# Kernel optimization log

Hardware: AMD Instinct MI355X
Metric: run time of the kernel (lower is better)

The kernel has to match this reference:

```python
import jax, jax.numpy as jnp
import numpy as np

NUM_CLASSES = 22
SKIP = 20            # skip_pixels: stride over flattened pixel index
N_STEPS = 200        # discretized steps along each voting ray
STEP = 4.0           # pixels per ray step
INLIER_T = 0.9       # inlier_threshold on direction dot-product
LABEL_T = 500.0      # label_threshold: min #pixels of a class to be valid


def _hough_forward(label_2d, vertex_pred, extents, poses, meta_data):
    B, H, W = label_2d.shape
    C = NUM_CLASSES
    HW = H * W

    # ---- strided pixel sampling (skip_pixels) ----
    idx = jnp.arange(0, HW, SKIP)                      # [P]
    P = idx.shape[0]
    ys = (idx // W).astype(jnp.float32)                # [P]
    xs = (idx % W).astype(jnp.float32)
    labels = label_2d.reshape(B, HW)[:, idx].astype(jnp.int32)   # [B,P]
    vp = vertex_pred.reshape(B, HW, C, 3)[:, idx]                # [B,P,C,3]
    # pick each pixel's predicted (dx,dy,z) for its own class label
    sel = jnp.take_along_axis(
        vp, jnp.broadcast_to(labels[:, :, None, None], (B, P, 1, 3)), axis=2
    )[:, :, 0]                                                   # [B,P,3]
    d = sel[..., :2]
    dn = d / (jnp.linalg.norm(d, axis=-1, keepdims=True) + 1e-9)  # unit dir [B,P,2]
    z = sel[..., 2]                                               # [B,P]
    fg = labels > 0                                               # foreground mask

    # ---- ray voting into per-class Hough accumulator ----
    t = (jnp.arange(N_STEPS, dtype=jnp.float32) + 1.0) * STEP     # [T]
    cx = xs[None, :, None] + dn[..., 0:1] * t[None, None, :]      # [B,P,T]
    cy = ys[None, :, None] + dn[..., 1:2] * t[None, None, :]
    cxi = jnp.round(cx).astype(jnp.int32)
    cyi = jnp.round(cy).astype(jnp.int32)
    inb = (cxi >= 0) & (cxi < W) & (cyi >= 0) & (cyi < H) & fg[..., None]
    cxi = jnp.clip(cxi, 0, W - 1)
    cyi = jnp.clip(cyi, 0, H - 1)
    bidx = jnp.arange(B, dtype=jnp.int32)[:, None, None]
    flat = ((bidx * C + labels[:, :, None]) * H + cyi) * W + cxi  # [B,P,T]
    hough = jnp.zeros((B * C * HW,), jnp.float32)
    hough = hough.at[flat.reshape(-1)].add(inb.reshape(-1).astype(jnp.float32))
    hough = hough.reshape(B, C, H, W)

    # ---- per-class peak ----
    hflat = hough.reshape(B, C, HW)
    vmax = hflat.max(-1)                               # [B,C]
    pk = jnp.argmax(hflat, axis=-1).astype(jnp.int32)  # [B,C]
    pky = (pk // W).astype(jnp.float32)
    pkx = (pk % W).astype(jnp.float32)

    # ---- validity: enough labeled pixels for the class ----
    b2 = jnp.arange(B, dtype=jnp.int32)[:, None]
    counts = jnp.zeros((B, C), jnp.float32).at[
        jnp.broadcast_to(b2, (B, HW)).reshape(-1),
        label_2d.reshape(-1).astype(jnp.int32),
    ].add(1.0)                                          # [B,C] full-res pixel counts
    cls_ids = jnp.arange(C, dtype=jnp.float32)
    valid = (counts >= LABEL_T) & (cls_ids[None, :] > 0)  # [B,C]

    # ---- inlier selection + inlier-averaged depth ----
    cx_c = jnp.take_along_axis(pkx, labels, axis=1)    # [B,P] peak of pixel's class
    cy_c = jnp.take_along_axis(pky, labels, axis=1)
    dvec = jnp.stack([cx_c - xs[None, :], cy_c - ys[None, :]], axis=-1)
    dvec = dvec / (jnp.linalg.norm(dvec, axis=-1, keepdims=True) + 1e-9)
    dot = jnp.sum(dn * dvec, axis=-1)                  # [B,P]
    inl = (fg & (dot > INLIER_T)).astype(jnp.float32)  # [B,P]
    bP = jnp.broadcast_to(b2, (B, P)).reshape(-1)
    z_sum = jnp.zeros((B, C), jnp.float32).at[bP, labels.reshape(-1)].add((z * inl).reshape(-1))
    n_inl = jnp.zeros((B, C), jnp.float32).at[bP, labels.reshape(-1)].add(inl.reshape(-1))
    depth = z_sum / jnp.maximum(n_inl, 1.0)            # [B,C]
    z_safe = jnp.where(jnp.abs(depth) > 1e-3, depth, 1.0)

    # ---- bbox from extents + intrinsics ----
    fx = meta_data[:, 0:1]                             # [B,1]
    fy = meta_data[:, 4:5]
    diam = jnp.linalg.norm(extents, axis=-1)[None, :]  # [1,C]
    half_w = 0.5 * diam * fx / z_safe
    half_h = 0.5 * diam * fy / z_safe
    vmask = valid.astype(jnp.float32)
    rois = jnp.stack([
        jnp.broadcast_to(b2.astype(jnp.float32), (B, C)),
        jnp.broadcast_to(cls_ids[None, :], (B, C)),
        pkx - half_w, pky - half_h, pkx + half_w, pky + half_h,
        vmax,
    ], axis=-1) * vmask[..., None]                     # [B,C,7]

    # ---- pose init: identity quaternion + backprojected translation ----
    Kinv = meta_data[:, 9:18].reshape(B, 3, 3)
    hom = jnp.stack([pkx, pky, jnp.ones_like(pkx)], axis=-1)      # [B,C,3]
    ray = jnp.einsum('bij,bcj->bci', Kinv, hom)
    T = depth[..., None] * ray                                    # [B,C,3]
    quat = jnp.broadcast_to(jnp.array([1.0, 0.0, 0.0, 0.0], jnp.float32), (B, C, 4))
    pose_out = jnp.concatenate([quat, T], axis=-1) * vmask[..., None]  # [B,C,7]

    return jnp.concatenate([rois, pose_out], axis=-1)  # [B,C,14]


def setup_inputs() -> dict:
    key = jax.random.key(0)
    k1, k2, k3 = jax.random.split(key, 3)
    B, H, W = 2, 480, 640
    label_2d = jax.random.randint(k1, (B, H, W), 0, NUM_CLASSES, dtype=jnp.int32)
    vertex_pred = jax.random.normal(k2, (B, H, W, 3 * NUM_CLASSES), dtype=jnp.float32)
    extents = jax.random.uniform(k3, (NUM_CLASSES, 3), minval=0.05, maxval=0.3, dtype=jnp.float32)
    poses = jnp.zeros((B, 13), jnp.float32)
    K = np.array([[1066.778, 0, 312.9869], [0, 1067.487, 241.3109], [0, 0, 1]], dtype=np.float32)
    Kinv = np.linalg.pinv(K).astype(np.float32)
    md = np.zeros((B, 48), np.float32)
    md[:, 0:9] = K.flatten()
    md[:, 9:18] = Kinv.flatten()
    meta_data = jnp.asarray(md)
    return {"label_2d": label_2d, "vertex_pred": vertex_pred, "extents": extents,
            "poses": poses, "meta_data": meta_data}


def reference(label_2d, vertex_pred, extents, poses, meta_data):
    return _hough_forward(label_2d, vertex_pred, extents, poses, meta_data)
```

## Files before the change

kernel.cpp:

```cpp
#include <hip/hip_runtime.h>
#include <math.h>

#define C_      22
#define SKIP_   20
#define NSTEP_  200
#define STEP_   4.0f
#define INL_T_  0.9f
#define LAB_T_  500
#define B_      2
#define H_      480
#define W_      640
#define HW_     (H_ * W_)
#define P_      (HW_ / SKIP_)

#define TS_       64
#define TILES_X_  (W_ / TS_)
#define TILES_Y_  (H_ / TS_)
#define NTILES_Y_ 8
#define NTILES_   (TILES_X_ * NTILES_Y_)
#define NPLANES_  (B_ * (C_ - 1))
#define NPT_      (NPLANES_ * NTILES_)
#define CAP_      1024

#define SUB_A_    4
#define SEG_LEN_  (NSTEP_ / SUB_A_)
#define PA_BLOCKS_    ((B_ * P_ * SUB_A_) / 256)
#define COUNT_BLOCKS_ ((B_ * HW_) / 256)

__device__ __forceinline__ void emit_run(unsigned int* cnt, uint4* lists, int pt,
                                         int xi, int yi, int i0, int i1,
                                         float dnx, float dny) {
    unsigned slot = atomicAdd(&cnt[pt], 1u);
    if (slot < CAP_) {
        uint4 r;
        r.x = (unsigned)xi | ((unsigned)yi << 16);
        r.y = (unsigned)i0 | ((unsigned)i1 << 8);
        r.z = __float_as_uint(dnx);
        r.w = __float_as_uint(dny);
        lists[(size_t)pt * CAP_ + slot] = r;
    }
}

__global__ __launch_bounds__(256) void binray_count_kernel(const int* __restrict__ label,
                                                           const float* __restrict__ vp,
                                                           unsigned int* __restrict__ cnt,
                                                           uint4* __restrict__ lists,
                                                           int* __restrict__ counts) {
    if (blockIdx.x < PA_BLOCKS_) {
        int tid = blockIdx.x * 256 + threadIdx.x;
        int pt  = tid >> 2;
        int sub = tid & 3;
        int b   = pt / P_;
        int pi  = pt - b * P_;
        int idx = pi * SKIP_;
        int lab = label[b * HW_ + idx];
        if (lab <= 0) return;
        int xi = idx % W_, yi = idx / W_;
        float xs = (float)xi, ys = (float)yi;
        const float* s = vp + ((size_t)(b * HW_ + idx) * (C_ * 3)) + lab * 3;
        float dx = s[0], dy = s[1];
        float nrm = sqrtf(__fadd_rn(__fmul_rn(dx, dx), __fmul_rn(dy, dy))) + 1e-9f;
        float dnx = dx / nrm, dny = dy / nrm;
        int base = (b * (C_ - 1) + (lab - 1)) * NTILES_;
        int curTile = -1, runStart = 0;
        int iBeg = sub * SEG_LEN_, iEnd = iBeg + SEG_LEN_;
        for (int i = iBeg; i < iEnd; ++i) {
            float t = (float)(i + 1) * STEP_;
            float cx = __fadd_rn(xs, __fmul_rn(dnx, t));
            float cy = __fadd_rn(ys, __fmul_rn(dny, t));
            float cxr = rintf(cx);
            float cyr = rintf(cy);
            int tile = -1;
            if (cxr >= 0.0f && cxr <= (float)(W_ - 1) && cyr >= 0.0f && cyr <= (float)(H_ - 1))
                tile = (((int)cyr) >> 6) * TILES_X_ + (((int)cxr) >> 6);
            if (tile != curTile) {
                if (curTile >= 0)
                    emit_run(cnt, lists, base + curTile, xi, yi, runStart, i - 1, dnx, dny);
                curTile = tile;
                runStart = i;
            }
        }
        if (curTile >= 0)
            emit_run(cnt, lists, base + curTile, xi, yi, runStart, iEnd - 1, dnx, dny);
    } else {
        __shared__ int h[C_];
        int cb  = blockIdx.x - PA_BLOCKS_;
        const int bpb = HW_ / 256;
        int b   = cb / bpb;
        int off = (cb % bpb) * 256 + threadIdx.x;
        if (threadIdx.x < C_) h[threadIdx.x] = 0;
        __syncthreads();
        int lab = label[b * HW_ + off];
        atomicAdd(&h[lab], 1);
        __syncthreads();
        if (threadIdx.x < C_) {
            int v = h[threadIdx.x];
            if (v) atomicAdd(&counts[b * C_ + threadIdx.x], v);
        }
    }
}

__global__ __launch_bounds__(256) void raster_argmax_kernel(const unsigned int* __restrict__ cnt,
                                                            const uint4* __restrict__ lists,
                                                            unsigned long long* __restrict__ key) {
    __shared__ unsigned int tile[TS_ * TS_];
    __shared__ unsigned int sv[256];
    __shared__ int          si[256];
    int ptile = blockIdx.x;
    int p  = ptile / NTILES_;
    int tl = ptile % NTILES_;
    int b = p / (C_ - 1);
    int c = p % (C_ - 1) + 1;
    int x0 = (tl % TILES_X_) * TS_;
    int y0 = (tl / TILES_X_) * TS_;
    for (int j = threadIdx.x; j < TS_ * TS_; j += 256) tile[j] = 0u;
    __syncthreads();
    int n = (int)cnt[ptile];
    if (n > CAP_) n = CAP_;
    const uint4* lst = lists + (size_t)ptile * CAP_;
    int wave = threadIdx.x >> 6, lane = threadIdx.x & 63;
    for (int r = wave; r < n; r += 4) {
        uint4 rec = lst[r];
        int i0 = (int)(rec.y & 0xFFu), i1 = (int)((rec.y >> 8) & 0xFFu);
        int i = i0 + lane;
        if (i <= i1) {
            float xs = (float)(rec.x & 0xFFFFu);
            float ys = (float)(rec.x >> 16);
            float dnx = __uint_as_float(rec.z);
            float dny = __uint_as_float(rec.w);
            float t = (float)(i + 1) * STEP_;
            float cx = __fadd_rn(xs, __fmul_rn(dnx, t));
            float cy = __fadd_rn(ys, __fmul_rn(dny, t));
            int lx = (int)rintf(cx) - x0;
            int ly = (int)rintf(cy) - y0;
            atomicAdd(&tile[ly * TS_ + lx], 1u);
        }
    }
    __syncthreads();
    int start = threadIdx.x * 16;
    unsigned bv = tile[start];
    int bloc = start;
    #pragma unroll
    for (int j = 1; j < 16; ++j) {
        unsigned v = tile[start + j];
        if (v > bv) { bv = v; bloc = start + j; }
    }
    sv[threadIdx.x] = bv; si[threadIdx.x] = bloc;
    __syncthreads();
    for (int s = 128; s > 0; s >>= 1) {
        if (threadIdx.x < s) {
            unsigned ov = sv[threadIdx.x + s]; int oi = si[threadIdx.x + s];
            if (ov > sv[threadIdx.x] || (ov == sv[threadIdx.x] && oi < si[threadIdx.x])) {
                sv[threadIdx.x] = ov; si[threadIdx.x] = oi;
            }
        }
        __syncthreads();
    }
    if (threadIdx.x == 0) {
        int ly = si[0] >> 6, lx = si[0] & 63;
        unsigned gidx = (unsigned)((y0 + ly) * W_ + (x0 + lx));
        unsigned long long k = ((unsigned long long)sv[0] << 32)
                             | (unsigned long long)(0xFFFFFFFFu - gidx);
        atomicMax(&key[b * C_ + c], k);
    }
}

__global__ __launch_bounds__(256) void inlier_kernel(const int* __restrict__ label,
                                                     const float* __restrict__ vp,
                                                     const unsigned long long* __restrict__ key,
                                                     float* __restrict__ z_sum,
                                                     float* __restrict__ n_inl) {
    __shared__ float zs[C_];
    __shared__ float ns[C_];
    const int bpb = P_ / 256;
    int b  = blockIdx.x / bpb;
    int pi = (blockIdx.x % bpb) * 256 + threadIdx.x;
    if (threadIdx.x < C_) { zs[threadIdx.x] = 0.0f; ns[threadIdx.x] = 0.0f; }
    __syncthreads();
    int idx = pi * SKIP_;
    int lab = label[b * HW_ + idx];
    if (lab > 0) {
        float ys = (float)(idx / W_);
        float xs = (float)(idx % W_);
        const float* s = vp + ((size_t)(b * HW_ + idx) * (C_ * 3)) + lab * 3;
        float dx = s[0], dy = s[1], z = s[2];
        float nrm = sqrtf(__fadd_rn(__fmul_rn(dx, dx), __fmul_rn(dy, dy))) + 1e-9f;
        float dnx = dx / nrm, dny = dy / nrm;
        unsigned long long k = key[b * C_ + lab];
        int pkv = (int)(0xFFFFFFFFu - (unsigned int)(k & 0xFFFFFFFFull));
        float pkx = (float)(pkv % W_), pky = (float)(pkv / W_);
        float dvx = __fsub_rn(pkx, xs), dvy = __fsub_rn(pky, ys);
        float nrm2 = sqrtf(__fadd_rn(__fmul_rn(dvx, dvx), __fmul_rn(dvy, dvy))) + 1e-9f;
        dvx /= nrm2; dvy /= nrm2;
        float dot = __fadd_rn(__fmul_rn(dnx, dvx), __fmul_rn(dny, dvy));
        if (dot > INL_T_) {
            atomicAdd(&zs[lab], z);
            atomicAdd(&ns[lab], 1.0f);
        }
    }
    __syncthreads();
    if (threadIdx.x < C_) {
        if (ns[threadIdx.x] != 0.0f) {
            atomicAdd(&z_sum[b * C_ + threadIdx.x], zs[threadIdx.x]);
            atomicAdd(&n_inl[b * C_ + threadIdx.x], ns[threadIdx.x]);
        }
    }
}

__global__ __launch_bounds__(64) void finalize_kernel(const int* __restrict__ counts,
                                                      const unsigned long long* __restrict__ key,
                                                      const float* __restrict__ z_sum,
                                                      const float* __restrict__ n_inl,
                                                      const float* __restrict__ extents,
                                                      const float* __restrict__ meta,
                                                      float* __restrict__ out) {
    int t = threadIdx.x;
    if (t >= B_ * C_) return;
    int b = t / C_, c = t % C_;
    float* o = out + t * 14;
    bool valid = (counts[t] >= LAB_T_) && (c > 0);
    if (!valid) {
        #pragma unroll
        for (int k = 0; k < 14; ++k) o[k] = 0.0f;
        return;
    }
    float depth = z_sum[t] / fmaxf(n_inl[t], 1.0f);
    float z_safe = (fabsf(depth) > 0.001f) ? depth : 1.0f;
    float fx = meta[b * 48 + 0];
    float fy = meta[b * 48 + 4];
    const float* e = extents + c * 3;
    float diam = sqrtf(e[0]*e[0] + e[1]*e[1] + e[2]*e[2]);
    unsigned long long k = key[t];
    float vmax = (float)(unsigned int)(k >> 32);
    int pkv = (int)(0xFFFFFFFFu - (unsigned int)(k & 0xFFFFFFFFull));
    float pkx = (float)(pkv % W_), pky = (float)(pkv / W_);
    float half_w = ((0.5f * diam) * fx) / z_safe;
    float half_h = ((0.5f * diam) * fy) / z_safe;
    o[0] = (float)b;
    o[1] = (float)c;
    o[2] = pkx - half_w;
    o[3] = pky - half_h;
    o[4] = pkx + half_w;
    o[5] = pky + half_h;
    o[6] = vmax;
    const float* Ki = meta + b * 48 + 9;
    float rx = Ki[0]*pkx + Ki[1]*pky + Ki[2];
    float ry = Ki[3]*pkx + Ki[4]*pky + Ki[5];
    float rz = Ki[6]*pkx + Ki[7]*pky + Ki[8];
    o[7]  = 1.0f;
    o[8]  = 0.0f;
    o[9]  = 0.0f;
    o[10] = 0.0f;
    o[11] = depth * rx;
    o[12] = depth * ry;
    o[13] = depth * rz;
}

extern "C" void kernel_launch(void* const* d_in, const int* in_sizes, int n_in,
                              void* d_out, int out_size, void* d_ws, size_t ws_size,
                              hipStream_t stream) {
    const int*   label   = (const int*)d_in[0];
    const float* vp      = (const float*)d_in[1];
    const float* extents = (const float*)d_in[2];
    const float* meta    = (const float*)d_in[4];
    float* out = (float*)d_out;

    char* ws = (char*)d_ws;
    size_t off = 0;
    unsigned int* cnt = (unsigned int*)(ws + off);          off += NPT_ * sizeof(unsigned int);
    unsigned long long* key = (unsigned long long*)(ws + off); off += B_ * C_ * sizeof(unsigned long long);
    int*   counts = (int*)(ws + off);   off += B_ * C_ * sizeof(int);
    float* z_sum  = (float*)(ws + off); off += B_ * C_ * sizeof(float);
    float* n_inl  = (float*)(ws + off); off += B_ * C_ * sizeof(float);
    size_t zero_bytes = off;
    uint4* lists = (uint4*)(ws + off);

    hipMemsetAsync(d_ws, 0, zero_bytes, stream);

    binray_count_kernel<<<PA_BLOCKS_ + COUNT_BLOCKS_, 256, 0, stream>>>(label, vp, cnt, lists, counts);
    raster_argmax_kernel<<<NPT_, 256, 0, stream>>>(cnt, lists, key);
    inlier_kernel<<<(B_ * P_) / 256, 256, 0, stream>>>(label, vp, key, z_sum, n_inl);
    finalize_kernel<<<1, 64, 0, stream>>>(counts, key, z_sum, n_inl, extents, meta, out);
}
```

Before: 288.1 us.

## Fuse memset and four kernels into one cooperative persistent kernel with grid syncs

Replaces the memset and the four separate launches (ray binning plus label counting, tile raster argmax, inlier accumulation, finalize) with one cooperative kernel of 512 persistent blocks. The blocks zero the workspace themselves and separate the phases with grid.sync. This removes launch and inter-kernel gaps, at the cost of grid barriers and a fixed block count that limits parallelism in the binning phase. The raster phase also changes from 64-lane waves per record to 32-lane groups with a strided loop, and the argmax scan changes from contiguous to strided shared-memory reads.

```diff
diff --git a/kernel.cpp b/kernel.cpp
--- a/kernel.cpp
+++ b/kernel.cpp
@@ -1,5 +1,8 @@
 #include <hip/hip_runtime.h>
+#include <hip/hip_cooperative_groups.h>
 #include <math.h>
+
+namespace cg = cooperative_groups;
 
 #define C_      22
 #define SKIP_   20
@@ -15,7 +18,6 @@
 
 #define TS_       64
 #define TILES_X_  (W_ / TS_)
-#define TILES_Y_  (H_ / TS_)
 #define NTILES_Y_ 8
 #define NTILES_   (TILES_X_ * NTILES_Y_)
 #define NPLANES_  (B_ * (C_ - 1))
@@ -26,6 +28,8 @@
 #define SEG_LEN_  (NSTEP_ / SUB_A_)
 #define PA_BLOCKS_    ((B_ * P_ * SUB_A_) / 256)
 #define COUNT_BLOCKS_ ((B_ * HW_) / 256)
+#define NB_       512
+#define ZERO_WORDS_ 13660
 
 __device__ __forceinline__ void emit_run(unsigned int* cnt, uint4* lists, int pt,
                                          int xi, int yi, int i0, int i1,
@@ -41,219 +45,226 @@
     }
 }
 
-__global__ __launch_bounds__(256) void binray_count_kernel(const int* __restrict__ label,
-                                                           const float* __restrict__ vp,
-                                                           unsigned int* __restrict__ cnt,
-                                                           uint4* __restrict__ lists,
-                                                           int* __restrict__ counts) {
-    if (blockIdx.x < PA_BLOCKS_) {
-        int tid = blockIdx.x * 256 + threadIdx.x;
-        int pt  = tid >> 2;
-        int sub = tid & 3;
-        int b   = pt / P_;
-        int pi  = pt - b * P_;
-        int idx = pi * SKIP_;
-        int lab = label[b * HW_ + idx];
-        if (lab <= 0) return;
-        int xi = idx % W_, yi = idx / W_;
-        float xs = (float)xi, ys = (float)yi;
-        const float* s = vp + ((size_t)(b * HW_ + idx) * (C_ * 3)) + lab * 3;
-        float dx = s[0], dy = s[1];
-        float nrm = sqrtf(__fadd_rn(__fmul_rn(dx, dx), __fmul_rn(dy, dy))) + 1e-9f;
-        float dnx = dx / nrm, dny = dy / nrm;
-        int base = (b * (C_ - 1) + (lab - 1)) * NTILES_;
-        int curTile = -1, runStart = 0;
-        int iBeg = sub * SEG_LEN_, iEnd = iBeg + SEG_LEN_;
-        for (int i = iBeg; i < iEnd; ++i) {
-            float t = (float)(i + 1) * STEP_;
-            float cx = __fadd_rn(xs, __fmul_rn(dnx, t));
-            float cy = __fadd_rn(ys, __fmul_rn(dny, t));
-            float cxr = rintf(cx);
-            float cyr = rintf(cy);
-            int tile = -1;
-            if (cxr >= 0.0f && cxr <= (float)(W_ - 1) && cyr >= 0.0f && cyr <= (float)(H_ - 1))
-                tile = (((int)cyr) >> 6) * TILES_X_ + (((int)cxr) >> 6);
-            if (tile != curTile) {
-                if (curTile >= 0)
-                    emit_run(cnt, lists, base + curTile, xi, yi, runStart, i - 1, dnx, dny);
-                curTile = tile;
-                runStart = i;
-            }
-        }
-        if (curTile >= 0)
-            emit_run(cnt, lists, base + curTile, xi, yi, runStart, iEnd - 1, dnx, dny);
-    } else {
-        __shared__ int h[C_];
-        int cb  = blockIdx.x - PA_BLOCKS_;
-        const int bpb = HW_ / 256;
-        int b   = cb / bpb;
-        int off = (cb % bpb) * 256 + threadIdx.x;
-        if (threadIdx.x < C_) h[threadIdx.x] = 0;
-        __syncthreads();
-        int lab = label[b * HW_ + off];
-        atomicAdd(&h[lab], 1);
-        __syncthreads();
-        if (threadIdx.x < C_) {
-            int v = h[threadIdx.x];
-            if (v) atomicAdd(&counts[b * C_ + threadIdx.x], v);
-        }
-    }
-}
-
-__global__ __launch_bounds__(256) void raster_argmax_kernel(const unsigned int* __restrict__ cnt,
-                                                            const uint4* __restrict__ lists,
-                                                            unsigned long long* __restrict__ key) {
+__global__ __launch_bounds__(256) void fused_kernel(
+        const int* __restrict__ label, const float* __restrict__ vp,
+        const float* __restrict__ extents, const float* __restrict__ meta,
+        float* __restrict__ out,
+        unsigned int* __restrict__ cnt, uint4* __restrict__ lists,
+        int* __restrict__ counts, unsigned long long* __restrict__ key,
+        float* __restrict__ z_sum, float* __restrict__ n_inl,
+        unsigned int* __restrict__ zero_base) {
+    cg::grid_group grid = cg::this_grid();
     __shared__ unsigned int tile[TS_ * TS_];
     __shared__ unsigned int sv[256];
     __shared__ int          si[256];
-    int ptile = blockIdx.x;
-    int p  = ptile / NTILES_;
-    int tl = ptile % NTILES_;
-    int b = p / (C_ - 1);
-    int c = p % (C_ - 1) + 1;
-    int x0 = (tl % TILES_X_) * TS_;
-    int y0 = (tl / TILES_X_) * TS_;
-    for (int j = threadIdx.x; j < TS_ * TS_; j += 256) tile[j] = 0u;
-    __syncthreads();
-    int n = (int)cnt[ptile];
-    if (n > CAP_) n = CAP_;
-    const uint4* lst = lists + (size_t)ptile * CAP_;
-    int wave = threadIdx.x >> 6, lane = threadIdx.x & 63;
-    for (int r = wave; r < n; r += 4) {
-        uint4 rec = lst[r];
-        int i0 = (int)(rec.y & 0xFFu), i1 = (int)((rec.y >> 8) & 0xFFu);
-        int i = i0 + lane;
-        if (i <= i1) {
+    __shared__ int   h[C_];
+    __shared__ float zs[C_], ns[C_];
+
+    int gtid = blockIdx.x * 256 + threadIdx.x;
+    if (gtid < ZERO_WORDS_) zero_base[gtid] = 0u;
+    grid.sync();
+
+    for (int vb = blockIdx.x; vb < PA_BLOCKS_ + COUNT_BLOCKS_; vb += NB_) {
+        if (vb < PA_BLOCKS_) {
+            int tid = vb * 256 + threadIdx.x;
+            int pt  = tid >> 2;
+            int sub = tid & 3;
+            int b   = pt / P_;
+            int pi  = pt - b * P_;
+            int idx = pi * SKIP_;
+            int lab = label[b * HW_ + idx];
+            if (lab > 0) {
+                int xi = idx % W_, yi = idx / W_;
+                float xs = (float)xi, ys = (float)yi;
+                const float* s = vp + ((size_t)(b * HW_ + idx) * (C_ * 3)) + lab * 3;
+                float dx = s[0], dy = s[1];
+                float nrm = sqrtf(__fadd_rn(__fmul_rn(dx, dx), __fmul_rn(dy, dy))) + 1e-9f;
+                float dnx = dx / nrm, dny = dy / nrm;
+                int base = (b * (C_ - 1) + (lab - 1)) * NTILES_;
+                int curTile = -1, runStart = 0;
+                int iBeg = sub * SEG_LEN_, iEnd = iBeg + SEG_LEN_;
+                for (int i = iBeg; i < iEnd; ++i) {
+                    float t = (float)(i + 1) * STEP_;
+                    float cx = __fadd_rn(xs, __fmul_rn(dnx, t));
+                    float cy = __fadd_rn(ys, __fmul_rn(dny, t));
+                    float cxr = rintf(cx);
+                    float cyr = rintf(cy);
+                    int tl2 = -1;
+                    if (cxr >= 0.0f && cxr <= (float)(W_ - 1) && cyr >= 0.0f && cyr <= (float)(H_ - 1))
+                        tl2 = (((int)cyr) >> 6) * TILES_X_ + (((int)cxr) >> 6);
+                    if (tl2 != curTile) {
+                        if (curTile >= 0)
+                            emit_run(cnt, lists, base + curTile, xi, yi, runStart, i - 1, dnx, dny);
+                        curTile = tl2;
+                        runStart = i;
+                    }
+                }
+                if (curTile >= 0)
+                    emit_run(cnt, lists, base + curTile, xi, yi, runStart, iEnd - 1, dnx, dny);
+            }
+        } else {
+            int cb  = vb - PA_BLOCKS_;
+            const int bpb = HW_ / 256;
+            int b   = cb / bpb;
+            int off = (cb % bpb) * 256 + threadIdx.x;
+            if (threadIdx.x < C_) h[threadIdx.x] = 0;
+            __syncthreads();
+            int lab = label[b * HW_ + off];
+            atomicAdd(&h[lab], 1);
+            __syncthreads();
+            if (threadIdx.x < C_) {
+                int v = h[threadIdx.x];
+                if (v) atomicAdd(&counts[b * C_ + threadIdx.x], v);
+            }
+            __syncthreads();
+        }
+    }
+    grid.sync();
+
+    for (int pt = blockIdx.x; pt < NPT_; pt += NB_) {
+        {
+            uint4* t4 = (uint4*)tile;
+            #pragma unroll
+            for (int j = 0; j < 4; ++j)
+                t4[threadIdx.x + j * 256] = make_uint4(0u, 0u, 0u, 0u);
+        }
+        __syncthreads();
+        int p  = pt / NTILES_;
+        int tl = pt % NTILES_;
+        int b = p / (C_ - 1);
+        int c = p % (C_ - 1) + 1;
+        int x0 = (tl % TILES_X_) * TS_;
+        int y0 = (tl / TILES_X_) * TS_;
+        int n = (int)cnt[pt];
+        if (n > CAP_) n = CAP_;
+        const uint4* lst = lists + (size_t)pt * CAP_;
+        int hwv = threadIdx.x >> 5, ln = threadIdx.x & 31;
+        for (int r = hwv; r < n; r += 8) {
+            uint4 rec = lst[r];
+            int i0 = (int)(rec.y & 0xFFu), i1 = (int)((rec.y >> 8) & 0xFFu);
             float xs = (float)(rec.x & 0xFFFFu);
             float ys = (float)(rec.x >> 16);
             float dnx = __uint_as_float(rec.z);
             float dny = __uint_as_float(rec.w);
-            float t = (float)(i + 1) * STEP_;
-            float cx = __fadd_rn(xs, __fmul_rn(dnx, t));
-            float cy = __fadd_rn(ys, __fmul_rn(dny, t));
-            int lx = (int)rintf(cx) - x0;
-            int ly = (int)rintf(cy) - y0;
-            atomicAdd(&tile[ly * TS_ + lx], 1u);
-        }
-    }
-    __syncthreads();
-    int start = threadIdx.x * 16;
-    unsigned bv = tile[start];
-    int bloc = start;
-    #pragma unroll
-    for (int j = 1; j < 16; ++j) {
-        unsigned v = tile[start + j];
-        if (v > bv) { bv = v; bloc = start + j; }
-    }
-    sv[threadIdx.x] = bv; si[threadIdx.x] = bloc;
-    __syncthreads();
-    for (int s = 128; s > 0; s >>= 1) {
-        if (threadIdx.x < s) {
-            unsigned ov = sv[threadIdx.x + s]; int oi = si[threadIdx.x + s];
-            if (ov > sv[threadIdx.x] || (ov == sv[threadIdx.x] && oi < si[threadIdx.x])) {
-                sv[threadIdx.x] = ov; si[threadIdx.x] = oi;
-            }
-        }
-        __syncthreads();
-    }
-    if (threadIdx.x == 0) {
-        int ly = si[0] >> 6, lx = si[0] & 63;
-        unsigned gidx = (unsigned)((y0 + ly) * W_ + (x0 + lx));
-        unsigned long long k = ((unsigned long long)sv[0] << 32)
-                             | (unsigned long long)(0xFFFFFFFFu - gidx);
-        atomicMax(&key[b * C_ + c], k);
-    }
-}
-
-__global__ __launch_bounds__(256) void inlier_kernel(const int* __restrict__ label,
-                                                     const float* __restrict__ vp,
-                                                     const unsigned long long* __restrict__ key,
-                                                     float* __restrict__ z_sum,
-                                                     float* __restrict__ n_inl) {
-    __shared__ float zs[C_];
-    __shared__ float ns[C_];
-    const int bpb = P_ / 256;
-    int b  = blockIdx.x / bpb;
-    int pi = (blockIdx.x % bpb) * 256 + threadIdx.x;
-    if (threadIdx.x < C_) { zs[threadIdx.x] = 0.0f; ns[threadIdx.x] = 0.0f; }
-    __syncthreads();
-    int idx = pi * SKIP_;
-    int lab = label[b * HW_ + idx];
-    if (lab > 0) {
-        float ys = (float)(idx / W_);
-        float xs = (float)(idx % W_);
-        const float* s = vp + ((size_t)(b * HW_ + idx) * (C_ * 3)) + lab * 3;
-        float dx = s[0], dy = s[1], z = s[2];
-        float nrm = sqrtf(__fadd_rn(__fmul_rn(dx, dx), __fmul_rn(dy, dy))) + 1e-9f;
-        float dnx = dx / nrm, dny = dy / nrm;
-        unsigned long long k = key[b * C_ + lab];
-        int pkv = (int)(0xFFFFFFFFu - (unsigned int)(k & 0xFFFFFFFFull));
-        float pkx = (float)(pkv % W_), pky = (float)(pkv / W_);
-        float dvx = __fsub_rn(pkx, xs), dvy = __fsub_rn(pky, ys);
-        float nrm2 = sqrtf(__fadd_rn(__fmul_rn(dvx, dvx), __fmul_rn(dvy, dvy))) + 1e-9f;
-        dvx /= nrm2; dvy /= nrm2;
-        float dot = __fadd_rn(__fmul_rn(dnx, dvx), __fmul_rn(dny, dvy));
-        if (dot > INL_T_) {
-            atomicAdd(&zs[lab], z);
-            atomicAdd(&ns[lab], 1.0f);
-        }
-    }
-    __syncthreads();
-    if (threadIdx.x < C_) {
-        if (ns[threadIdx.x] != 0.0f) {
-            atomicAdd(&z_sum[b * C_ + threadIdx.x], zs[threadIdx.x]);
-            atomicAdd(&n_inl[b * C_ + threadIdx.x], ns[threadIdx.x]);
-        }
-    }
-}
-
-__global__ __launch_bounds__(64) void finalize_kernel(const int* __restrict__ counts,
-                                                      const unsigned long long* __restrict__ key,
-                                                      const float* __restrict__ z_sum,
-                                                      const float* __restrict__ n_inl,
-                                                      const float* __restrict__ extents,
-                                                      const float* __restrict__ meta,
-                                                      float* __restrict__ out) {
-    int t = threadIdx.x;
-    if (t >= B_ * C_) return;
-    int b = t / C_, c = t % C_;
-    float* o = out + t * 14;
-    bool valid = (counts[t] >= LAB_T_) && (c > 0);
-    if (!valid) {
+            for (int i = i0 + ln; i <= i1; i += 32) {
+                float t = (float)(i + 1) * STEP_;
+                float cx = __fadd_rn(xs, __fmul_rn(dnx, t));
+                float cy = __fadd_rn(ys, __fmul_rn(dny, t));
+                int lx = (int)rintf(cx) - x0;
+                int ly = (int)rintf(cy) - y0;
+                atomicAdd(&tile[ly * TS_ + lx], 1u);
+            }
+        }
+        __syncthreads();
+        unsigned bv = tile[threadIdx.x];
+        int bi = threadIdx.x;
         #pragma unroll
-        for (int k = 0; k < 14; ++k) o[k] = 0.0f;
-        return;
-    }
-    float depth = z_sum[t] / fmaxf(n_inl[t], 1.0f);
-    float z_safe = (fabsf(depth) > 0.001f) ? depth : 1.0f;
-    float fx = meta[b * 48 + 0];
-    float fy = meta[b * 48 + 4];
-    const float* e = extents + c * 3;
-    float diam = sqrtf(e[0]*e[0] + e[1]*e[1] + e[2]*e[2]);
-    unsigned long long k = key[t];
-    float vmax = (float)(unsigned int)(k >> 32);
-    int pkv = (int)(0xFFFFFFFFu - (unsigned int)(k & 0xFFFFFFFFull));
-    float pkx = (float)(pkv % W_), pky = (float)(pkv / W_);
-    float half_w = ((0.5f * diam) * fx) / z_safe;
-    float half_h = ((0.5f * diam) * fy) / z_safe;
-    o[0] = (float)b;
-    o[1] = (float)c;
-    o[2] = pkx - half_w;
-    o[3] = pky - half_h;
-    o[4] = pkx + half_w;
-    o[5] = pky + half_h;
-    o[6] = vmax;
-    const float* Ki = meta + b * 48 + 9;
-    float rx = Ki[0]*pkx + Ki[1]*pky + Ki[2];
-    float ry = Ki[3]*pkx + Ki[4]*pky + Ki[5];
-    float rz = Ki[6]*pkx + Ki[7]*pky + Ki[8];
-    o[7]  = 1.0f;
-    o[8]  = 0.0f;
-    o[9]  = 0.0f;
-    o[10] = 0.0f;
-    o[11] = depth * rx;
-    o[12] = depth * ry;
-    o[13] = depth * rz;
+        for (int j = 1; j < 16; ++j) {
+            int ix = threadIdx.x + j * 256;
+            unsigned v = tile[ix];
+            if (v > bv) { bv = v; bi = ix; }
+        }
+        sv[threadIdx.x] = bv; si[threadIdx.x] = bi;
+        __syncthreads();
+        for (int s = 128; s > 0; s >>= 1) {
+            if (threadIdx.x < s) {
+                unsigned ov = sv[threadIdx.x + s]; int oi = si[threadIdx.x + s];
+                if (ov > sv[threadIdx.x] || (ov == sv[threadIdx.x] && oi < si[threadIdx.x])) {
+                    sv[threadIdx.x] = ov; si[threadIdx.x] = oi;
+                }
+            }
+            __syncthreads();
+        }
+        if (threadIdx.x == 0) {
+            int ly = si[0] >> 6, lx = si[0] & 63;
+            unsigned gidx = (unsigned)((y0 + ly) * W_ + (x0 + lx));
+            unsigned long long k = ((unsigned long long)sv[0] << 32)
+                                 | (unsigned long long)(0xFFFFFFFFu - gidx);
+            atomicMax(&key[b * C_ + c], k);
+        }
+        __syncthreads();
+    }
+    grid.sync();
+
+    for (int vb = blockIdx.x; vb < (B_ * P_) / 256; vb += NB_) {
+        const int bpb = P_ / 256;
+        int b  = vb / bpb;
+        int pi = (vb % bpb) * 256 + threadIdx.x;
+        if (threadIdx.x < C_) { zs[threadIdx.x] = 0.0f; ns[threadIdx.x] = 0.0f; }
+        __syncthreads();
+        int idx = pi * SKIP_;
+        int lab = label[b * HW_ + idx];
+        if (lab > 0) {
+            float ys = (float)(idx / W_);
+            float xs = (float)(idx % W_);
+            const float* s = vp + ((size_t)(b * HW_ + idx) * (C_ * 3)) + lab * 3;
+            float dx = s[0], dy = s[1], z = s[2];
+            float nrm = sqrtf(__fadd_rn(__fmul_rn(dx, dx), __fmul_rn(dy, dy))) + 1e-9f;
+            float dnx = dx / nrm, dny = dy / nrm;
+            unsigned long long k = key[b * C_ + lab];
+            int pkv = (int)(0xFFFFFFFFu - (unsigned int)(k & 0xFFFFFFFFull));
+            float pkx = (float)(pkv % W_), pky = (float)(pkv / W_);
+            float dvx = __fsub_rn(pkx, xs), dvy = __fsub_rn(pky, ys);
+            float nrm2 = sqrtf(__fadd_rn(__fmul_rn(dvx, dvx), __fmul_rn(dvy, dvy))) + 1e-9f;
+            dvx /= nrm2; dvy /= nrm2;
+            float dot = __fadd_rn(__fmul_rn(dnx, dvx), __fmul_rn(dny, dvy));
+            if (dot > INL_T_) {
+                atomicAdd(&zs[lab], z);
+                atomicAdd(&ns[lab], 1.0f);
+            }
+        }
+        __syncthreads();
+        if (threadIdx.x < C_) {
+            if (ns[threadIdx.x] != 0.0f) {
+                atomicAdd(&z_sum[b * C_ + threadIdx.x], zs[threadIdx.x]);
+                atomicAdd(&n_inl[b * C_ + threadIdx.x], ns[threadIdx.x]);
+            }
+        }
+        __syncthreads();
+    }
+    grid.sync();
+
+    if (blockIdx.x == 0 && threadIdx.x < B_ * C_) {
+        int t = threadIdx.x;
+        int b = t / C_, c = t % C_;
+        float* o = out + t * 14;
+        bool valid = (counts[t] >= LAB_T_) && (c > 0);
+        if (!valid) {
+            #pragma unroll
+            for (int k2 = 0; k2 < 14; ++k2) o[k2] = 0.0f;
+        } else {
+            float depth = z_sum[t] / fmaxf(n_inl[t], 1.0f);
+            float z_safe = (fabsf(depth) > 0.001f) ? depth : 1.0f;
+            float fx = meta[b * 48 + 0];
+            float fy = meta[b * 48 + 4];
+            const float* e = extents + c * 3;
+            float diam = sqrtf(e[0]*e[0] + e[1]*e[1] + e[2]*e[2]);
+            unsigned long long k = key[t];
+            float vmax = (float)(unsigned int)(k >> 32);
+            int pkv = (int)(0xFFFFFFFFu - (unsigned int)(k & 0xFFFFFFFFull));
+            float pkx = (float)(pkv % W_), pky = (float)(pkv / W_);
+            float half_w = ((0.5f * diam) * fx) / z_safe;
+            float half_h = ((0.5f * diam) * fy) / z_safe;
+            o[0] = (float)b;
+            o[1] = (float)c;
+            o[2] = pkx - half_w;
+            o[3] = pky - half_h;
+            o[4] = pkx + half_w;
+            o[5] = pky + half_h;
+            o[6] = vmax;
+            const float* Ki = meta + b * 48 + 9;
+            float rx = Ki[0]*pkx + Ki[1]*pky + Ki[2];
+            float ry = Ki[3]*pkx + Ki[4]*pky + Ki[5];
+            float rz = Ki[6]*pkx + Ki[7]*pky + Ki[8];
+            o[7]  = 1.0f;
+            o[8]  = 0.0f;
+            o[9]  = 0.0f;
+            o[10] = 0.0f;
+            o[11] = depth * rx;
+            o[12] = depth * ry;
+            o[13] = depth * rz;
+        }
+    }
 }
 
 extern "C" void kernel_launch(void* const* d_in, const int* in_sizes, int n_in,
@@ -267,18 +278,16 @@
 
     char* ws = (char*)d_ws;
     size_t off = 0;
-    unsigned int* cnt = (unsigned int*)(ws + off);          off += NPT_ * sizeof(unsigned int);
+    unsigned int* cnt = (unsigned int*)(ws + off);             off += NPT_ * sizeof(unsigned int);
     unsigned long long* key = (unsigned long long*)(ws + off); off += B_ * C_ * sizeof(unsigned long long);
     int*   counts = (int*)(ws + off);   off += B_ * C_ * sizeof(int);
     float* z_sum  = (float*)(ws + off); off += B_ * C_ * sizeof(float);
     float* n_inl  = (float*)(ws + off); off += B_ * C_ * sizeof(float);
-    size_t zero_bytes = off;
     uint4* lists = (uint4*)(ws + off);
-
-    hipMemsetAsync(d_ws, 0, zero_bytes, stream);
-
-    binray_count_kernel<<<PA_BLOCKS_ + COUNT_BLOCKS_, 256, 0, stream>>>(label, vp, cnt, lists, counts);
-    raster_argmax_kernel<<<NPT_, 256, 0, stream>>>(cnt, lists, key);
-    inlier_kernel<<<(B_ * P_) / 256, 256, 0, stream>>>(label, vp, key, z_sum, n_inl);
-    finalize_kernel<<<1, 64, 0, stream>>>(counts, key, z_sum, n_inl, extents, meta, out);
+    unsigned int* zero_base = (unsigned int*)d_ws;
+
+    void* args[] = { (void*)&label, (void*)&vp, (void*)&extents, (void*)&meta, (void*)&out,
+                     (void*)&cnt, (void*)&lists, (void*)&counts, (void*)&key,
+                     (void*)&z_sum, (void*)&n_inl, (void*)&zero_base };
+    hipLaunchCooperativeKernel((void*)fused_kernel, dim3(NB_), dim3(256), args, 0, stream);
 }
```

Result: slower. 472.4 us (+63.9%).

## Split rays into 8 segments, pack 16-bit tile bins, skip empty tiles

Applied to the files above, without the earlier changes.

Each ray is now split across 8 threads instead of 4, and a thread stops stepping once its ray has left the image. The raster kernel returns early for tiles that received no runs. It packs two 16-bit counters per shared-memory word, halving the tile's size and zeroing cost, and processes runs with half-waves that loop over steps. The key array is now initialised to a sentinel inside the count kernel instead of by the memset, and the list capacity doubles. Packed 16-bit counters could overflow on very dense bins, and early-exit blocks still leave key at its sentinel for planes with no hits.

```diff
diff --git a/kernel.cpp b/kernel.cpp
--- a/kernel.cpp
+++ b/kernel.cpp
@@ -15,17 +15,19 @@
 
 #define TS_       64
 #define TILES_X_  (W_ / TS_)
-#define TILES_Y_  (H_ / TS_)
 #define NTILES_Y_ 8
 #define NTILES_   (TILES_X_ * NTILES_Y_)
 #define NPLANES_  (B_ * (C_ - 1))
 #define NPT_      (NPLANES_ * NTILES_)
-#define CAP_      1024
-
-#define SUB_A_    4
+#define CAP_      2048
+
+#define SUB_A_    8
 #define SEG_LEN_  (NSTEP_ / SUB_A_)
 #define PA_BLOCKS_    ((B_ * P_ * SUB_A_) / 256)
 #define COUNT_BLOCKS_ ((B_ * HW_) / 256)
+#define INL_BLOCKS_   ((B_ * P_) / 256)
+
+#define KEY_INIT_ 0x00000000FFFFFFFFull
 
 __device__ __forceinline__ void emit_run(unsigned int* cnt, uint4* lists, int pt,
                                          int xi, int yi, int i0, int i1,
@@ -45,11 +47,12 @@
                                                            const float* __restrict__ vp,
                                                            unsigned int* __restrict__ cnt,
                                                            uint4* __restrict__ lists,
-                                                           int* __restrict__ counts) {
+                                                           int* __restrict__ counts,
+                                                           unsigned long long* __restrict__ key) {
     if (blockIdx.x < PA_BLOCKS_) {
         int tid = blockIdx.x * 256 + threadIdx.x;
-        int pt  = tid >> 2;
-        int sub = tid & 3;
+        int pt  = tid >> 3;
+        int sub = tid & 7;
         int b   = pt / P_;
         int pi  = pt - b * P_;
         int idx = pi * SKIP_;
@@ -63,6 +66,7 @@
         float dnx = dx / nrm, dny = dy / nrm;
         int base = (b * (C_ - 1) + (lab - 1)) * NTILES_;
         int curTile = -1, runStart = 0;
+        bool entered = false;
         int iBeg = sub * SEG_LEN_, iEnd = iBeg + SEG_LEN_;
         for (int i = iBeg; i < iEnd; ++i) {
             float t = (float)(i + 1) * STEP_;
@@ -70,21 +74,25 @@
             float cy = __fadd_rn(ys, __fmul_rn(dny, t));
             float cxr = rintf(cx);
             float cyr = rintf(cy);
-            int tile = -1;
+            int tl2 = -1;
             if (cxr >= 0.0f && cxr <= (float)(W_ - 1) && cyr >= 0.0f && cyr <= (float)(H_ - 1))
-                tile = (((int)cyr) >> 6) * TILES_X_ + (((int)cxr) >> 6);
-            if (tile != curTile) {
+                tl2 = (((int)cyr) >> 6) * TILES_X_ + (((int)cxr) >> 6);
+            if (tl2 != curTile) {
                 if (curTile >= 0)
                     emit_run(cnt, lists, base + curTile, xi, yi, runStart, i - 1, dnx, dny);
-                curTile = tile;
+                curTile = tl2;
                 runStart = i;
             }
+            if (tl2 >= 0) entered = true;
+            else if (entered) break;
         }
         if (curTile >= 0)
             emit_run(cnt, lists, base + curTile, xi, yi, runStart, iEnd - 1, dnx, dny);
     } else {
         __shared__ int h[C_];
         int cb  = blockIdx.x - PA_BLOCKS_;
+        if (cb == 0 && threadIdx.x < B_ * C_)
+            key[threadIdx.x] = KEY_INIT_;
         const int bpb = HW_ / 256;
         int b   = cb / bpb;
         int off = (cb % bpb) * 256 + threadIdx.x;
@@ -103,49 +111,61 @@
 __global__ __launch_bounds__(256) void raster_argmax_kernel(const unsigned int* __restrict__ cnt,
                                                             const uint4* __restrict__ lists,
                                                             unsigned long long* __restrict__ key) {
-    __shared__ unsigned int tile[TS_ * TS_];
+    __shared__ unsigned int tile[TS_ * TS_ / 2];
     __shared__ unsigned int sv[256];
     __shared__ int          si[256];
-    int ptile = blockIdx.x;
-    int p  = ptile / NTILES_;
-    int tl = ptile % NTILES_;
+    int pt = blockIdx.x;
+    int n = (int)cnt[pt];
+    if (n == 0) return;
+    if (n > CAP_) n = CAP_;
+    {
+        uint4* t4 = (uint4*)tile;
+        t4[threadIdx.x]       = make_uint4(0u, 0u, 0u, 0u);
+        t4[threadIdx.x + 256] = make_uint4(0u, 0u, 0u, 0u);
+    }
+    __syncthreads();
+    int p  = pt / NTILES_;
+    int tl = pt % NTILES_;
     int b = p / (C_ - 1);
     int c = p % (C_ - 1) + 1;
     int x0 = (tl % TILES_X_) * TS_;
     int y0 = (tl / TILES_X_) * TS_;
-    for (int j = threadIdx.x; j < TS_ * TS_; j += 256) tile[j] = 0u;
-    __syncthreads();
-    int n = (int)cnt[ptile];
-    if (n > CAP_) n = CAP_;
-    const uint4* lst = lists + (size_t)ptile * CAP_;
-    int wave = threadIdx.x >> 6, lane = threadIdx.x & 63;
-    for (int r = wave; r < n; r += 4) {
+    const uint4* lst = lists + (size_t)pt * CAP_;
+    int hwv = threadIdx.x >> 5, ln = threadIdx.x & 31;
+    for (int r = hwv; r < n; r += 8) {
         uint4 rec = lst[r];
         int i0 = (int)(rec.y & 0xFFu), i1 = (int)((rec.y >> 8) & 0xFFu);
-        int i = i0 + lane;
-        if (i <= i1) {
-            float xs = (float)(rec.x & 0xFFFFu);
-            float ys = (float)(rec.x >> 16);
-            float dnx = __uint_as_float(rec.z);
-            float dny = __uint_as_float(rec.w);
+        float xs = (float)(rec.x & 0xFFFFu);
+        float ys = (float)(rec.x >> 16);
+        float dnx = __uint_as_float(rec.z);
+        float dny = __uint_as_float(rec.w);
+        for (int i = i0 + ln; i <= i1; i += 32) {
             float t = (float)(i + 1) * STEP_;
             float cx = __fadd_rn(xs, __fmul_rn(dnx, t));
             float cy = __fadd_rn(ys, __fmul_rn(dny, t));
             int lx = (int)rintf(cx) - x0;
             int ly = (int)rintf(cy) - y0;
-            atomicAdd(&tile[ly * TS_ + lx], 1u);
-        }
-    }
-    __syncthreads();
-    int start = threadIdx.x * 16;
-    unsigned bv = tile[start];
-    int bloc = start;
+            int cell = ly * TS_ + lx;
+            atomicAdd(&tile[cell >> 1], 1u << ((cell & 1) * 16));
+        }
+    }
+    __syncthreads();
+    unsigned bv = 0u; int bi = 0;
+    {
+        unsigned w0 = tile[threadIdx.x];
+        bv = w0 & 0xFFFFu; bi = threadIdx.x * 2;
+        unsigned hi = w0 >> 16;
+        if (hi > bv) { bv = hi; bi = threadIdx.x * 2 + 1; }
+    }
     #pragma unroll
-    for (int j = 1; j < 16; ++j) {
-        unsigned v = tile[start + j];
-        if (v > bv) { bv = v; bloc = start + j; }
-    }
-    sv[threadIdx.x] = bv; si[threadIdx.x] = bloc;
+    for (int j = 1; j < 8; ++j) {
+        int ix = threadIdx.x + j * 256;
+        unsigned w = tile[ix];
+        unsigned lo = w & 0xFFFFu, hi = w >> 16;
+        if (lo > bv) { bv = lo; bi = ix * 2; }
+        if (hi > bv) { bv = hi; bi = ix * 2 + 1; }
+    }
+    sv[threadIdx.x] = bv; si[threadIdx.x] = bi;
     __syncthreads();
     for (int s = 128; s > 0; s >>= 1) {
         if (threadIdx.x < s) {
@@ -221,7 +241,7 @@
     bool valid = (counts[t] >= LAB_T_) && (c > 0);
     if (!valid) {
         #pragma unroll
-        for (int k = 0; k < 14; ++k) o[k] = 0.0f;
+        for (int k2 = 0; k2 < 14; ++k2) o[k2] = 0.0f;
         return;
     }
     float depth = z_sum[t] / fmaxf(n_inl[t], 1.0f);
@@ -267,18 +287,21 @@
 
     char* ws = (char*)d_ws;
     size_t off = 0;
-    unsigned int* cnt = (unsigned int*)(ws + off);          off += NPT_ * sizeof(unsigned int);
-    unsigned long long* key = (unsigned long long*)(ws + off); off += B_ * C_ * sizeof(unsigned long long);
+    unsigned int* cnt = (unsigned int*)(ws + off);  off += NPT_ * sizeof(unsigned int);
     int*   counts = (int*)(ws + off);   off += B_ * C_ * sizeof(int);
     float* z_sum  = (float*)(ws + off); off += B_ * C_ * sizeof(float);
     float* n_inl  = (float*)(ws + off); off += B_ * C_ * sizeof(float);
     size_t zero_bytes = off;
+    off = (off + 15) & ~(size_t)15;
+    unsigned long long* key = (unsigned long long*)(ws + off);
+    off += B_ * C_ * sizeof(unsigned long long);
+    off = (off + 15) & ~(size_t)15;
     uint4* lists = (uint4*)(ws + off);
 
     hipMemsetAsync(d_ws, 0, zero_bytes, stream);
 
-    binray_count_kernel<<<PA_BLOCKS_ + COUNT_BLOCKS_, 256, 0, stream>>>(label, vp, cnt, lists, counts);
+    binray_count_kernel<<<PA_BLOCKS_ + COUNT_BLOCKS_, 256, 0, stream>>>(label, vp, cnt, lists, counts, key);
     raster_argmax_kernel<<<NPT_, 256, 0, stream>>>(cnt, lists, key);
-    inlier_kernel<<<(B_ * P_) / 256, 256, 0, stream>>>(label, vp, key, z_sum, n_inl);
+    inlier_kernel<<<INL_BLOCKS_, 256, 0, stream>>>(label, vp, key, z_sum, n_inl);
     finalize_kernel<<<1, 64, 0, stream>>>(counts, key, z_sum, n_inl, extents, meta, out);
 }
```

Result: faster. 269.5 us (-6.5%).
